# Optimization experiments

Measured on AMD Instinct MI355X. Metric: run time of the kernel, lower is better.

Reference implementation:

```python
import jax, jax.numpy as jnp
import numpy as np
from jax import lax

B, C_IN, C_OUT, H, W, K, PAD = 4, 64, 64, 96, 96, 3, 1
K2 = K * K


def setup_inputs() -> dict:
    key = jax.random.key(0)
    k1, k2, k3, k4, k5 = jax.random.split(key, 5)
    x = jax.random.normal(k1, (B, C_IN, H, W), jnp.float32)
    offset = jax.random.normal(k2, (B, 2 * K2, H, W), jnp.float32)
    weight = jax.random.normal(k3, (C_OUT, C_IN, K, K), jnp.float32) * 0.05
    mask_weight = jax.random.normal(k4, (K2, C_IN, K, K), jnp.float32) * 0.05
    mask_bias = jax.random.normal(k5, (K2,), jnp.float32) * 0.05
    return {"x": x, "offset": offset, "weight": weight,
            "mask_weight": mask_weight, "mask_bias": mask_bias}


def _deform_conv2d(x, offset, weight, mask):
    # torchvision ordering: per kernel tap k, offset[:, 2k] is dy, offset[:, 2k+1] is dx
    off_y = offset[:, 0::2]  # [B, K2, H, W]
    off_x = offset[:, 1::2]
    ky, kx = jnp.meshgrid(jnp.arange(K), jnp.arange(K), indexing="ij")
    ky = ky.reshape(K2).astype(x.dtype)
    kx = kx.reshape(K2).astype(x.dtype)
    hh = jnp.arange(H, dtype=x.dtype)
    ww = jnp.arange(W, dtype=x.dtype)
    base_y = hh[None, :, None] - PAD + ky[:, None, None]   # [K2, H, 1]
    base_x = ww[None, None, :] - PAD + kx[:, None, None]   # [K2, 1, W]
    py = base_y[None] + off_y                               # [B, K2, H, W]
    px = base_x[None] + off_x

    y0 = jnp.floor(py)
    x0 = jnp.floor(px)
    wy = py - y0   # bilinear weights
    wx = px - x0
    y0i = y0.astype(jnp.int32)
    x0i = x0.astype(jnp.int32)

    x_flat = x.reshape(B, C_IN, H * W)

    def gather(yy, xx):
        valid = (yy >= 0) & (yy < H) & (xx >= 0) & (xx < W)
        idx = jnp.clip(yy, 0, H - 1) * W + jnp.clip(xx, 0, W - 1)  # [B,K2,H,W]
        idx_f = idx.reshape(B, -1)
        v = jax.vmap(lambda xf, i: xf[:, i])(x_flat, idx_f)  # [B, C, K2*H*W]
        v = v.reshape(B, C_IN, K2, H, W)
        return v * valid[:, None].astype(v.dtype)

    v00 = gather(y0i, x0i)
    v01 = gather(y0i, x0i + 1)
    v10 = gather(y0i + 1, x0i)
    v11 = gather(y0i + 1, x0i + 1)

    wy_ = wy[:, None]  # [B,1,K2,H,W]
    wx_ = wx[:, None]
    sampled = (v00 * (1 - wy_) * (1 - wx_) + v01 * (1 - wy_) * wx_
               + v10 * wy_ * (1 - wx_) + v11 * wy_ * wx_)
    sampled = sampled * mask[:, None]  # modulate by sigmoid mask

    w2 = weight.reshape(C_OUT, C_IN, K2)
    return jnp.einsum("bckhw,ock->bohw", sampled, w2)


def reference(x, offset, weight, mask_weight, mask_bias):
    mask_logits = lax.conv_general_dilated(
        x, mask_weight, window_strides=(1, 1), padding=[(PAD, PAD), (PAD, PAD)],
        dimension_numbers=("NCHW", "OIHW", "NCHW"))
    mask = jax.nn.sigmoid(mask_logits + mask_bias[None, :, None, None])
    return _deform_conv2d(x, offset, weight, mask)
```

## Files before the change

### kernel.cpp

```cpp
#include <hip/hip_runtime.h>
#include <math.h>

#define BB 4
#define CI 64
#define CO 64
#define HH 96
#define WW 96
#define HW (HH*WW)
#define K2 9
#define NT (HW/64)
#define TPX 32
#define NTT (HW/TPX)
#define PADC 1

typedef __attribute__((ext_vector_type(8))) short short8;
typedef __attribute__((ext_vector_type(4))) float float4v;

#define XT_USHORTS ((size_t)BB*HW*64)
#define WF_USHORTS (18*64*32)
#define MWF_USHORTS (18*16*32)

__device__ __forceinline__ float bf2f(short s) {
    return __uint_as_float(((unsigned int)(unsigned short)s) << 16);
}
__device__ __forceinline__ short f2bf(float f) {
    unsigned int u = __float_as_uint(f);
    u = (u + 0x7fffu + ((u >> 16) & 1u)) >> 16;
    return (short)u;
}

__device__ __forceinline__ void unswz64(int bid, int* b, int* tile) {
    int g = bid & 7, r = bid >> 3;
    *b = g & 3;
    *tile = (g >> 2) * 72 + r;
}
__device__ __forceinline__ void unswz32(int bid, int* b, int* tile) {
    int g = bid & 7, r = bid >> 3;
    *b = g & 3;
    *tile = (g >> 2) * 144 + r;
}

__global__ __launch_bounds__(256) void prep_kernel(const float* __restrict__ x,
                                                   const float* __restrict__ wgt,
                                                   const float* __restrict__ mw,
                                                   unsigned short* __restrict__ xT,
                                                   unsigned short* __restrict__ Wf,
                                                   unsigned short* __restrict__ MWf) {
    __shared__ unsigned short ts[64][72];
    int t = threadIdx.x;
    if (blockIdx.x < BB * NT) {
        int b, tl; unswz64(blockIdx.x, &b, &tl);
        int p0 = tl * 64;
        const float* xb = x + (size_t)b * CI * HW + p0;
        int pq = t & 15, cg = t >> 4;
        #pragma unroll
        for (int i = 0; i < 4; i++) {
            int c = cg + i * 16;
            float4v v = *(const float4v*)(xb + (size_t)c * HW + pq * 4);
            ts[pq * 4 + 0][c] = (unsigned short)f2bf(v[0]);
            ts[pq * 4 + 1][c] = (unsigned short)f2bf(v[1]);
            ts[pq * 4 + 2][c] = (unsigned short)f2bf(v[2]);
            ts[pq * 4 + 3][c] = (unsigned short)f2bf(v[3]);
        }
        __syncthreads();
        int px = t >> 2, cq = t & 3;
        unsigned short* xo = xT + ((size_t)b * HW + p0 + px) * 64 + cq * 16;
        *(short8*)xo       = *(const short8*)&ts[px][cq * 16];
        *(short8*)(xo + 8) = *(const short8*)&ts[px][cq * 16 + 8];
    } else {
        int i = (blockIdx.x - BB * NT) * 256 + t;
        if (i < WF_USHORTS) {
            int frag = i >> 11;
            int o = (i >> 5) & 63;
            int tt = i & 31;
            int k = frag >> 1, cc = frag & 1;
            int c = cc * 32 + tt;
            Wf[i] = (unsigned short)f2bf(wgt[o * 576 + c * 9 + k]);
        } else if (i < WF_USHORTS + MWF_USHORTS) {
            int e = i - WF_USHORTS;
            int frag = e >> 9;
            int m = (e >> 5) & 15;
            int tt = e & 31;
            int q = frag >> 1, cc = frag & 1;
            int c = cc * 32 + tt;
            MWf[e] = (m < 9) ? (unsigned short)f2bf(mw[m * 576 + c * 9 + q]) : 0;
        }
    }
}

__global__ __launch_bounds__(256) void fused_kernel(const float* __restrict__ off,
                                                    const float* __restrict__ mbias,
                                                    const unsigned short* __restrict__ xT,
                                                    const unsigned short* __restrict__ Wf,
                                                    const unsigned short* __restrict__ MWf,
                                                    float* __restrict__ out) {
    __shared__ float s_mred[2][K2][TPX];
    __shared__ int   s_idx[K2][4][TPX];
    __shared__ float s_w[K2][4][TPX];
    __shared__ float s_part[2][16][64];

    int t = threadIdx.x;
    int lane = t & 63, wv = t >> 6;
    int pg = wv & 1, ch = wv >> 1;
    int n = lane & 15, quad = lane >> 4;
    int b, tl; unswz32(blockIdx.x, &b, &tl);
    int p0 = tl * TPX;
    int pxl = pg * 16 + n;
    int p = p0 + pxl;
    int h = p / WW, wc = p % WW;
    const unsigned short* xTb = xT + (size_t)b * HW * 64;
    int cbase = ch * 32 + quad * 8;

    {
        float4v macc = {0.f, 0.f, 0.f, 0.f};
        #pragma unroll
        for (int q = 0; q < 9; q++) {
            int hh = h + q / 3 - 1, ww2 = wc + q % 3 - 1;
            bool valid = (hh >= 0) && (hh < HH) && (ww2 >= 0) && (ww2 < WW);
            int nidx = valid ? (hh * WW + ww2) : 0;
            short8 bfrag = {0, 0, 0, 0, 0, 0, 0, 0};
            if (valid) bfrag = *(const short8*)(xTb + (size_t)nidx * 64 + cbase);
            short8 afrag = *(const short8*)(MWf + ((size_t)((q * 2 + ch) * 16 + n)) * 32 + quad * 8);
            macc = __builtin_amdgcn_mfma_f32_16x16x32_bf16(afrag, bfrag, macc, 0, 0, 0);
        }
        #pragma unroll
        for (int r = 0; r < 4; r++) {
            int row = quad * 4 + r;
            if (row < 9) s_mred[ch][row][pxl] = macc[r];
        }
    }
    __syncthreads();

    for (int e = t; e < K2 * TPX; e += 256) {
        int k = e >> 5, pe = e & 31;
        int pp = p0 + pe;
        int hh0 = pp / WW, ww0 = pp % WW;
        int ky = k / 3, kx = k % 3;
        float oy = off[((size_t)b * 2 * K2 + 2 * k) * HW + pp];
        float ox = off[((size_t)b * 2 * K2 + 2 * k + 1) * HW + pp];
        float s = s_mred[0][k][pe] + s_mred[1][k][pe] + mbias[k];
        float m = 1.f / (1.f + expf(-s));
        float py = (float)(hh0 - PADC + ky) + oy;
        float pxf = (float)(ww0 - PADC + kx) + ox;
        float y0f = floorf(py), x0f = floorf(pxf);
        float wy = py - y0f, wx = pxf - x0f;
        int y0 = (int)y0f, x0 = (int)x0f;
        int y1 = y0 + 1, x1 = x0 + 1;
        int y0c = min(max(y0, 0), HH - 1), y1c = min(max(y1, 0), HH - 1);
        int x0c = min(max(x0, 0), WW - 1), x1c = min(max(x1, 0), WW - 1);
        bool vy0 = (y0 >= 0) && (y0 < HH), vy1 = (y1 >= 0) && (y1 < HH);
        bool vx0 = (x0 >= 0) && (x0 < WW), vx1 = (x1 >= 0) && (x1 < WW);
        float w00 = (1.f - wy) * (1.f - wx) * m; if (!(vy0 && vx0)) w00 = 0.f;
        float w01 = (1.f - wy) * wx * m;         if (!(vy0 && vx1)) w01 = 0.f;
        float w10 = wy * (1.f - wx) * m;         if (!(vy1 && vx0)) w10 = 0.f;
        float w11 = wy * wx * m;                 if (!(vy1 && vx1)) w11 = 0.f;
        s_idx[k][0][pe] = y0c * WW + x0c;
        s_idx[k][1][pe] = y0c * WW + x1c;
        s_idx[k][2][pe] = y1c * WW + x0c;
        s_idx[k][3][pe] = y1c * WW + x1c;
        s_w[k][0][pe] = w00; s_w[k][1][pe] = w01;
        s_w[k][2][pe] = w10; s_w[k][3][pe] = w11;
    }
    __syncthreads();

    float4v acc0 = {0.f, 0.f, 0.f, 0.f};
    float4v acc1 = {0.f, 0.f, 0.f, 0.f};
    float4v acc2 = {0.f, 0.f, 0.f, 0.f};
    float4v acc3 = {0.f, 0.f, 0.f, 0.f};
    const unsigned short* xq = xTb + cbase;

    #pragma unroll
    for (int k = 0; k < 9; k++) {
        int i0 = s_idx[k][0][pxl], i1 = s_idx[k][1][pxl];
        int i2 = s_idx[k][2][pxl], i3 = s_idx[k][3][pxl];
        float w0 = s_w[k][0][pxl], w1 = s_w[k][1][pxl];
        float w2 = s_w[k][2][pxl], w3 = s_w[k][3][pxl];
        short8 u0 = *(const short8*)(xq + (size_t)i0 * 64);
        short8 u1 = *(const short8*)(xq + (size_t)i1 * 64);
        short8 u2 = *(const short8*)(xq + (size_t)i2 * 64);
        short8 u3 = *(const short8*)(xq + (size_t)i3 * 64);
        short8 bfrag;
        #pragma unroll
        for (int j = 0; j < 8; j++) {
            float v = bf2f(u0[j]) * w0 + bf2f(u1[j]) * w1 +
                      bf2f(u2[j]) * w2 + bf2f(u3[j]) * w3;
            bfrag[j] = f2bf(v);
        }
        const unsigned short* wp = Wf + (size_t)((k * 2 + ch) * 64) * 32 + quad * 8;
        short8 a0 = *(const short8*)(wp + (0 * 16 + n) * 32);
        short8 a1 = *(const short8*)(wp + (1 * 16 + n) * 32);
        short8 a2 = *(const short8*)(wp + (2 * 16 + n) * 32);
        short8 a3 = *(const short8*)(wp + (3 * 16 + n) * 32);
        acc0 = __builtin_amdgcn_mfma_f32_16x16x32_bf16(a0, bfrag, acc0, 0, 0, 0);
        acc1 = __builtin_amdgcn_mfma_f32_16x16x32_bf16(a1, bfrag, acc1, 0, 0, 0);
        acc2 = __builtin_amdgcn_mfma_f32_16x16x32_bf16(a2, bfrag, acc2, 0, 0, 0);
        acc3 = __builtin_amdgcn_mfma_f32_16x16x32_bf16(a3, bfrag, acc3, 0, 0, 0);
    }

    if (ch == 1) {
        #pragma unroll
        for (int r = 0; r < 4; r++) {
            s_part[pg][0 * 4 + r][lane] = acc0[r];
            s_part[pg][1 * 4 + r][lane] = acc1[r];
            s_part[pg][2 * 4 + r][lane] = acc2[r];
            s_part[pg][3 * 4 + r][lane] = acc3[r];
        }
    }
    __syncthreads();
    if (ch == 0) {
        float* ob = out + (size_t)b * CO * HW + p0 + pxl;
        #pragma unroll
        for (int r = 0; r < 4; r++) {
            ob[(size_t)(0 * 16 + quad * 4 + r) * HW] = acc0[r] + s_part[pg][0 * 4 + r][lane];
            ob[(size_t)(1 * 16 + quad * 4 + r) * HW] = acc1[r] + s_part[pg][1 * 4 + r][lane];
            ob[(size_t)(2 * 16 + quad * 4 + r) * HW] = acc2[r] + s_part[pg][2 * 4 + r][lane];
            ob[(size_t)(3 * 16 + quad * 4 + r) * HW] = acc3[r] + s_part[pg][3 * 4 + r][lane];
        }
    }
}

extern "C" void kernel_launch(void* const* d_in, const int* in_sizes, int n_in,
                              void* d_out, int out_size, void* d_ws, size_t ws_size,
                              hipStream_t stream) {
    const float* x   = (const float*)d_in[0];
    const float* off = (const float*)d_in[1];
    const float* wgt = (const float*)d_in[2];
    const float* mw  = (const float*)d_in[3];
    const float* mb  = (const float*)d_in[4];
    float* out = (float*)d_out;

    unsigned short* xT  = (unsigned short*)d_ws;
    unsigned short* Wf  = xT + XT_USHORTS;
    unsigned short* MWf = Wf + WF_USHORTS;

    int prep_grid = BB * NT + (WF_USHORTS + MWF_USHORTS + 255) / 256;
    hipLaunchKernelGGL(prep_kernel, dim3(prep_grid), dim3(256), 0, stream,
                       x, wgt, mw, xT, Wf, MWf);
    hipLaunchKernelGGL(fused_kernel, dim3(BB * NTT), dim3(256), 0, stream,
                       off, mb, xT, Wf, MWf, out);
}
```

Before: 112.1 us.

## Split kernel taps across waves with 16-pixel tiles and smaller prep tiles

```diff
diff --git a/kernel.cpp b/kernel.cpp
--- a/kernel.cpp
+++ b/kernel.cpp
@@ -8,9 +8,9 @@
 #define WW 96
 #define HW (HH*WW)
 #define K2 9
-#define NT (HW/64)
-#define TPX 32
+#define TPX 16
 #define NTT (HW/TPX)
+#define NTP 288
 #define PADC 1
 
 typedef __attribute__((ext_vector_type(8))) short short8;
@@ -29,10 +29,10 @@
     return (short)u;
 }
 
-__device__ __forceinline__ void unswz64(int bid, int* b, int* tile) {
+__device__ __forceinline__ void unswz16(int bid, int* b, int* tile) {
     int g = bid & 7, r = bid >> 3;
     *b = g & 3;
-    *tile = (g >> 2) * 72 + r;
+    *tile = (g >> 2) * 288 + r;
 }
 __device__ __forceinline__ void unswz32(int bid, int* b, int* tile) {
     int g = bid & 7, r = bid >> 3;
@@ -40,22 +40,23 @@
     *tile = (g >> 2) * 144 + r;
 }
 
+#define PBASE (BB*NTP)
 __global__ __launch_bounds__(256) void prep_kernel(const float* __restrict__ x,
                                                    const float* __restrict__ wgt,
                                                    const float* __restrict__ mw,
                                                    unsigned short* __restrict__ xT,
                                                    unsigned short* __restrict__ Wf,
                                                    unsigned short* __restrict__ MWf) {
-    __shared__ unsigned short ts[64][72];
+    __shared__ unsigned short ts[32][72];
     int t = threadIdx.x;
-    if (blockIdx.x < BB * NT) {
-        int b, tl; unswz64(blockIdx.x, &b, &tl);
-        int p0 = tl * 64;
+    if (blockIdx.x < PBASE) {
+        int b, tl; unswz32(blockIdx.x, &b, &tl);
+        int p0 = tl * 32;
         const float* xb = x + (size_t)b * CI * HW + p0;
-        int pq = t & 15, cg = t >> 4;
-        #pragma unroll
-        for (int i = 0; i < 4; i++) {
-            int c = cg + i * 16;
+        int c0 = t >> 3, pq = t & 7;
+        #pragma unroll
+        for (int i = 0; i < 2; i++) {
+            int c = c0 + i * 32;
             float4v v = *(const float4v*)(xb + (size_t)c * HW + pq * 4);
             ts[pq * 4 + 0][c] = (unsigned short)f2bf(v[0]);
             ts[pq * 4 + 1][c] = (unsigned short)f2bf(v[1]);
@@ -63,12 +64,11 @@
             ts[pq * 4 + 3][c] = (unsigned short)f2bf(v[3]);
         }
         __syncthreads();
-        int px = t >> 2, cq = t & 3;
-        unsigned short* xo = xT + ((size_t)b * HW + p0 + px) * 64 + cq * 16;
-        *(short8*)xo       = *(const short8*)&ts[px][cq * 16];
-        *(short8*)(xo + 8) = *(const short8*)&ts[px][cq * 16 + 8];
+        int px = t >> 3, cq = t & 7;
+        unsigned short* xo = xT + ((size_t)b * HW + p0 + px) * 64 + cq * 8;
+        *(short8*)xo = *(const short8*)&ts[px][cq * 8];
     } else {
-        int i = (blockIdx.x - BB * NT) * 256 + t;
+        int i = (blockIdx.x - PBASE) * 256 + t;
         if (i < WF_USHORTS) {
             int frag = i >> 11;
             int o = (i >> 5) & 63;
@@ -88,57 +88,60 @@
     }
 }
 
-__global__ __launch_bounds__(256) void fused_kernel(const float* __restrict__ off,
-                                                    const float* __restrict__ mbias,
-                                                    const unsigned short* __restrict__ xT,
-                                                    const unsigned short* __restrict__ Wf,
-                                                    const unsigned short* __restrict__ MWf,
-                                                    float* __restrict__ out) {
-    __shared__ float s_mred[2][K2][TPX];
+__global__ __launch_bounds__(256, 6) void fused_kernel(const float* __restrict__ off,
+                                                       const float* __restrict__ mbias,
+                                                       const unsigned short* __restrict__ xT,
+                                                       const unsigned short* __restrict__ Wf,
+                                                       const unsigned short* __restrict__ MWf,
+                                                       float* __restrict__ out) {
+    __shared__ float s_mred[2][2][K2][TPX];
     __shared__ int   s_idx[K2][4][TPX];
     __shared__ float s_w[K2][4][TPX];
-    __shared__ float s_part[2][16][64];
+    __shared__ float s_part[3][16][64];
 
     int t = threadIdx.x;
     int lane = t & 63, wv = t >> 6;
-    int pg = wv & 1, ch = wv >> 1;
+    int ch = wv & 1, tg = wv >> 1;
     int n = lane & 15, quad = lane >> 4;
-    int b, tl; unswz32(blockIdx.x, &b, &tl);
+    int b, tl; unswz16(blockIdx.x, &b, &tl);
     int p0 = tl * TPX;
-    int pxl = pg * 16 + n;
-    int p = p0 + pxl;
+    int p = p0 + n;
     int h = p / WW, wc = p % WW;
     const unsigned short* xTb = xT + (size_t)b * HW * 64;
     int cbase = ch * 32 + quad * 8;
 
     {
         float4v macc = {0.f, 0.f, 0.f, 0.f};
-        #pragma unroll
-        for (int q = 0; q < 9; q++) {
-            int hh = h + q / 3 - 1, ww2 = wc + q % 3 - 1;
-            bool valid = (hh >= 0) && (hh < HH) && (ww2 >= 0) && (ww2 < WW);
-            int nidx = valid ? (hh * WW + ww2) : 0;
-            short8 bfrag = {0, 0, 0, 0, 0, 0, 0, 0};
-            if (valid) bfrag = *(const short8*)(xTb + (size_t)nidx * 64 + cbase);
-            short8 afrag = *(const short8*)(MWf + ((size_t)((q * 2 + ch) * 16 + n)) * 32 + quad * 8);
-            macc = __builtin_amdgcn_mfma_f32_16x16x32_bf16(afrag, bfrag, macc, 0, 0, 0);
-        }
+#define PHASE_A(QB, QE)                                                          \
+        _Pragma("unroll")                                                        \
+        for (int q = QB; q < QE; q++) {                                          \
+            int hh = h + q / 3 - 1, ww2 = wc + q % 3 - 1;                        \
+            bool valid = (hh >= 0) && (hh < HH) && (ww2 >= 0) && (ww2 < WW);     \
+            int nidx = valid ? (hh * WW + ww2) : 0;                              \
+            short8 bfrag = {0, 0, 0, 0, 0, 0, 0, 0};                             \
+            if (valid) bfrag = *(const short8*)(xTb + (size_t)nidx * 64 + cbase);\
+            short8 afrag = *(const short8*)(MWf +                                \
+                ((size_t)((q * 2 + ch) * 16 + n)) * 32 + quad * 8);              \
+            macc = __builtin_amdgcn_mfma_f32_16x16x32_bf16(afrag, bfrag, macc, 0, 0, 0); \
+        }
+        if (tg == 0) { PHASE_A(0, 5) } else { PHASE_A(5, 9) }
         #pragma unroll
         for (int r = 0; r < 4; r++) {
             int row = quad * 4 + r;
-            if (row < 9) s_mred[ch][row][pxl] = macc[r];
+            if (row < 9) s_mred[ch][tg][row][n] = macc[r];
         }
     }
     __syncthreads();
 
-    for (int e = t; e < K2 * TPX; e += 256) {
-        int k = e >> 5, pe = e & 31;
+    if (t < K2 * TPX) {
+        int k = t >> 4, pe = t & 15;
         int pp = p0 + pe;
         int hh0 = pp / WW, ww0 = pp % WW;
         int ky = k / 3, kx = k % 3;
         float oy = off[((size_t)b * 2 * K2 + 2 * k) * HW + pp];
         float ox = off[((size_t)b * 2 * K2 + 2 * k + 1) * HW + pp];
-        float s = s_mred[0][k][pe] + s_mred[1][k][pe] + mbias[k];
+        float s = s_mred[0][0][k][pe] + s_mred[0][1][k][pe] +
+                  s_mred[1][0][k][pe] + s_mred[1][1][k][pe] + mbias[k];
         float m = 1.f / (1.f + expf(-s));
         float py = (float)(hh0 - PADC + ky) + oy;
         float pxf = (float)(ww0 - PADC + kx) + ox;
@@ -169,52 +172,59 @@
     float4v acc3 = {0.f, 0.f, 0.f, 0.f};
     const unsigned short* xq = xTb + cbase;
 
-    #pragma unroll
-    for (int k = 0; k < 9; k++) {
-        int i0 = s_idx[k][0][pxl], i1 = s_idx[k][1][pxl];
-        int i2 = s_idx[k][2][pxl], i3 = s_idx[k][3][pxl];
-        float w0 = s_w[k][0][pxl], w1 = s_w[k][1][pxl];
-        float w2 = s_w[k][2][pxl], w3 = s_w[k][3][pxl];
-        short8 u0 = *(const short8*)(xq + (size_t)i0 * 64);
-        short8 u1 = *(const short8*)(xq + (size_t)i1 * 64);
-        short8 u2 = *(const short8*)(xq + (size_t)i2 * 64);
-        short8 u3 = *(const short8*)(xq + (size_t)i3 * 64);
-        short8 bfrag;
-        #pragma unroll
-        for (int j = 0; j < 8; j++) {
-            float v = bf2f(u0[j]) * w0 + bf2f(u1[j]) * w1 +
-                      bf2f(u2[j]) * w2 + bf2f(u3[j]) * w3;
-            bfrag[j] = f2bf(v);
-        }
-        const unsigned short* wp = Wf + (size_t)((k * 2 + ch) * 64) * 32 + quad * 8;
-        short8 a0 = *(const short8*)(wp + (0 * 16 + n) * 32);
-        short8 a1 = *(const short8*)(wp + (1 * 16 + n) * 32);
-        short8 a2 = *(const short8*)(wp + (2 * 16 + n) * 32);
-        short8 a3 = *(const short8*)(wp + (3 * 16 + n) * 32);
-        acc0 = __builtin_amdgcn_mfma_f32_16x16x32_bf16(a0, bfrag, acc0, 0, 0, 0);
-        acc1 = __builtin_amdgcn_mfma_f32_16x16x32_bf16(a1, bfrag, acc1, 0, 0, 0);
-        acc2 = __builtin_amdgcn_mfma_f32_16x16x32_bf16(a2, bfrag, acc2, 0, 0, 0);
-        acc3 = __builtin_amdgcn_mfma_f32_16x16x32_bf16(a3, bfrag, acc3, 0, 0, 0);
-    }
-
-    if (ch == 1) {
+#define PHASE_C(KB, KE)                                                          \
+    _Pragma("unroll")                                                            \
+    for (int k = KB; k < KE; k++) {                                              \
+        int i0 = s_idx[k][0][n], i1 = s_idx[k][1][n];                            \
+        int i2 = s_idx[k][2][n], i3 = s_idx[k][3][n];                            \
+        float w0 = s_w[k][0][n], w1 = s_w[k][1][n];                              \
+        float w2 = s_w[k][2][n], w3 = s_w[k][3][n];                              \
+        short8 u0 = *(const short8*)(xq + (size_t)i0 * 64);                      \
+        short8 u1 = *(const short8*)(xq + (size_t)i1 * 64);                      \
+        short8 u2 = *(const short8*)(xq + (size_t)i2 * 64);                      \
+        short8 u3 = *(const short8*)(xq + (size_t)i3 * 64);                      \
+        short8 bfrag;                                                            \
+        _Pragma("unroll")                                                        \
+        for (int j = 0; j < 8; j++) {                                            \
+            float v = bf2f(u0[j]) * w0 + bf2f(u1[j]) * w1 +                      \
+                      bf2f(u2[j]) * w2 + bf2f(u3[j]) * w3;                       \
+            bfrag[j] = f2bf(v);                                                  \
+        }                                                                        \
+        const unsigned short* wp = Wf + (size_t)((k * 2 + ch) * 64) * 32 + quad * 8; \
+        short8 a0 = *(const short8*)(wp + (0 * 16 + n) * 32);                    \
+        short8 a1 = *(const short8*)(wp + (1 * 16 + n) * 32);                    \
+        short8 a2 = *(const short8*)(wp + (2 * 16 + n) * 32);                    \
+        short8 a3 = *(const short8*)(wp + (3 * 16 + n) * 32);                    \
+        acc0 = __builtin_amdgcn_mfma_f32_16x16x32_bf16(a0, bfrag, acc0, 0, 0, 0);\
+        acc1 = __builtin_amdgcn_mfma_f32_16x16x32_bf16(a1, bfrag, acc1, 0, 0, 0);\
+        acc2 = __builtin_amdgcn_mfma_f32_16x16x32_bf16(a2, bfrag, acc2, 0, 0, 0);\
+        acc3 = __builtin_amdgcn_mfma_f32_16x16x32_bf16(a3, bfrag, acc3, 0, 0, 0);\
+    }
+    if (tg == 0) { PHASE_C(0, 5) } else { PHASE_C(5, 9) }
+
+    if (wv != 0) {
         #pragma unroll
         for (int r = 0; r < 4; r++) {
-            s_part[pg][0 * 4 + r][lane] = acc0[r];
-            s_part[pg][1 * 4 + r][lane] = acc1[r];
-            s_part[pg][2 * 4 + r][lane] = acc2[r];
-            s_part[pg][3 * 4 + r][lane] = acc3[r];
+            s_part[wv - 1][0 * 4 + r][lane] = acc0[r];
+            s_part[wv - 1][1 * 4 + r][lane] = acc1[r];
+            s_part[wv - 1][2 * 4 + r][lane] = acc2[r];
+            s_part[wv - 1][3 * 4 + r][lane] = acc3[r];
         }
     }
     __syncthreads();
-    if (ch == 0) {
-        float* ob = out + (size_t)b * CO * HW + p0 + pxl;
+    if (wv == 0) {
+        float* ob = out + (size_t)b * CO * HW + p0 + n;
         #pragma unroll
         for (int r = 0; r < 4; r++) {
-            ob[(size_t)(0 * 16 + quad * 4 + r) * HW] = acc0[r] + s_part[pg][0 * 4 + r][lane];
-            ob[(size_t)(1 * 16 + quad * 4 + r) * HW] = acc1[r] + s_part[pg][1 * 4 + r][lane];
-            ob[(size_t)(2 * 16 + quad * 4 + r) * HW] = acc2[r] + s_part[pg][2 * 4 + r][lane];
-            ob[(size_t)(3 * 16 + quad * 4 + r) * HW] = acc3[r] + s_part[pg][3 * 4 + r][lane];
+            int j0 = 0 * 4 + r, j1 = 1 * 4 + r, j2 = 2 * 4 + r, j3 = 3 * 4 + r;
+            ob[(size_t)(0 * 16 + quad * 4 + r) * HW] =
+                acc0[r] + s_part[0][j0][lane] + s_part[1][j0][lane] + s_part[2][j0][lane];
+            ob[(size_t)(1 * 16 + quad * 4 + r) * HW] =
+                acc1[r] + s_part[0][j1][lane] + s_part[1][j1][lane] + s_part[2][j1][lane];
+            ob[(size_t)(2 * 16 + quad * 4 + r) * HW] =
+                acc2[r] + s_part[0][j2][lane] + s_part[1][j2][lane] + s_part[2][j2][lane];
+            ob[(size_t)(3 * 16 + quad * 4 + r) * HW] =
+                acc3[r] + s_part[0][j3][lane] + s_part[1][j3][lane] + s_part[2][j3][lane];
         }
     }
 }
@@ -233,7 +243,7 @@
     unsigned short* Wf  = xT + XT_USHORTS;
     unsigned short* MWf = Wf + WF_USHORTS;
 
-    int prep_grid = BB * NT + (WF_USHORTS + MWF_USHORTS + 255) / 256;
+    int prep_grid = PBASE + (WF_USHORTS + MWF_USHORTS + 255) / 256;
     hipLaunchKernelGGL(prep_kernel, dim3(prep_grid), dim3(256), 0, stream,
                        x, wgt, mw, xT, Wf, MWf);
     hipLaunchKernelGGL(fused_kernel, dim3(BB * NTT), dim3(256), 0, stream,
```

After: 106.8 us. 1.05x faster.

## Stage bf16 input halo window in LDS per 2D tile, drop transpose pass

Applied to the files above, without the earlier changes.

```diff
diff --git a/kernel.cpp b/kernel.cpp
--- a/kernel.cpp
+++ b/kernel.cpp
@@ -8,15 +8,24 @@
 #define WW 96
 #define HW (HH*WW)
 #define K2 9
-#define NT (HW/64)
-#define TPX 32
-#define NTT (HW/TPX)
 #define PADC 1
+
+#define TW 8
+#define TH 4
+#define TPXT (TW*TH)
+#define TBX (WW/TW)
+#define TBY (HH/TH)
+#define NTILB (TBX*TBY)
+#define NTILES (BB*NTILB)
+
+#define WR (TH+9)
+#define WC 20
+#define SREC 72
+#define NSLOT (WR*WC)
 
 typedef __attribute__((ext_vector_type(8))) short short8;
 typedef __attribute__((ext_vector_type(4))) float float4v;
 
-#define XT_USHORTS ((size_t)BB*HW*64)
 #define WF_USHORTS (18*64*32)
 #define MWF_USHORTS (18*16*32)
 
@@ -29,97 +38,101 @@
     return (short)u;
 }
 
-__device__ __forceinline__ void unswz64(int bid, int* b, int* tile) {
+__device__ __forceinline__ void unswz(int bid, int* b, int* ty, int* tx) {
     int g = bid & 7, r = bid >> 3;
     *b = g & 3;
-    *tile = (g >> 2) * 72 + r;
-}
-__device__ __forceinline__ void unswz32(int bid, int* b, int* tile) {
-    int g = bid & 7, r = bid >> 3;
-    *b = g & 3;
-    *tile = (g >> 2) * 144 + r;
-}
-
-__global__ __launch_bounds__(256) void prep_kernel(const float* __restrict__ x,
-                                                   const float* __restrict__ wgt,
+    int tile = (g >> 2) * 144 + r;
+    *ty = tile / TBX; *tx = tile % TBX;
+}
+
+__global__ __launch_bounds__(256) void pack_kernel(const float* __restrict__ wgt,
                                                    const float* __restrict__ mw,
-                                                   unsigned short* __restrict__ xT,
                                                    unsigned short* __restrict__ Wf,
                                                    unsigned short* __restrict__ MWf) {
-    __shared__ unsigned short ts[64][72];
-    int t = threadIdx.x;
-    if (blockIdx.x < BB * NT) {
-        int b, tl; unswz64(blockIdx.x, &b, &tl);
-        int p0 = tl * 64;
-        const float* xb = x + (size_t)b * CI * HW + p0;
-        int pq = t & 15, cg = t >> 4;
-        #pragma unroll
-        for (int i = 0; i < 4; i++) {
-            int c = cg + i * 16;
-            float4v v = *(const float4v*)(xb + (size_t)c * HW + pq * 4);
-            ts[pq * 4 + 0][c] = (unsigned short)f2bf(v[0]);
-            ts[pq * 4 + 1][c] = (unsigned short)f2bf(v[1]);
-            ts[pq * 4 + 2][c] = (unsigned short)f2bf(v[2]);
-            ts[pq * 4 + 3][c] = (unsigned short)f2bf(v[3]);
-        }
-        __syncthreads();
-        int px = t >> 2, cq = t & 3;
-        unsigned short* xo = xT + ((size_t)b * HW + p0 + px) * 64 + cq * 16;
-        *(short8*)xo       = *(const short8*)&ts[px][cq * 16];
-        *(short8*)(xo + 8) = *(const short8*)&ts[px][cq * 16 + 8];
-    } else {
-        int i = (blockIdx.x - BB * NT) * 256 + t;
-        if (i < WF_USHORTS) {
-            int frag = i >> 11;
-            int o = (i >> 5) & 63;
-            int tt = i & 31;
-            int k = frag >> 1, cc = frag & 1;
-            int c = cc * 32 + tt;
-            Wf[i] = (unsigned short)f2bf(wgt[o * 576 + c * 9 + k]);
-        } else if (i < WF_USHORTS + MWF_USHORTS) {
-            int e = i - WF_USHORTS;
-            int frag = e >> 9;
-            int m = (e >> 5) & 15;
-            int tt = e & 31;
-            int q = frag >> 1, cc = frag & 1;
-            int c = cc * 32 + tt;
-            MWf[e] = (m < 9) ? (unsigned short)f2bf(mw[m * 576 + c * 9 + q]) : 0;
-        }
-    }
-}
-
-__global__ __launch_bounds__(256) void fused_kernel(const float* __restrict__ off,
-                                                    const float* __restrict__ mbias,
-                                                    const unsigned short* __restrict__ xT,
-                                                    const unsigned short* __restrict__ Wf,
-                                                    const unsigned short* __restrict__ MWf,
-                                                    float* __restrict__ out) {
-    __shared__ float s_mred[2][K2][TPX];
-    __shared__ int   s_idx[K2][4][TPX];
-    __shared__ float s_w[K2][4][TPX];
-    __shared__ float s_part[2][16][64];
+    int i = blockIdx.x * 256 + threadIdx.x;
+    if (i < WF_USHORTS) {
+        int frag = i >> 11;
+        int o = (i >> 5) & 63;
+        int tt = i & 31;
+        int k = frag >> 1, cc = frag & 1;
+        int c = cc * 32 + tt;
+        Wf[i] = (unsigned short)f2bf(wgt[o * 576 + c * 9 + k]);
+    } else if (i < WF_USHORTS + MWF_USHORTS) {
+        int e = i - WF_USHORTS;
+        int frag = e >> 9;
+        int m = (e >> 5) & 15;
+        int tt = e & 31;
+        int q = frag >> 1, cc = frag & 1;
+        int c = cc * 32 + tt;
+        MWf[e] = (m < 9) ? (unsigned short)f2bf(mw[m * 576 + c * 9 + q]) : 0;
+    }
+}
+
+__global__ __launch_bounds__(256, 3) void fused_kernel(const float* __restrict__ x,
+                                                       const float* __restrict__ off,
+                                                       const float* __restrict__ mbias,
+                                                       const unsigned short* __restrict__ Wf,
+                                                       const unsigned short* __restrict__ MWf,
+                                                       float* __restrict__ out) {
+    __shared__ __align__(16) unsigned short win[NSLOT * SREC];
+    __shared__ float s_mred[2][K2][TPXT];
+    __shared__ int   s_idx[K2][4][TPXT];
+    __shared__ float s_w[K2][4][TPXT];
+    float* part = (float*)win;
 
     int t = threadIdx.x;
     int lane = t & 63, wv = t >> 6;
-    int pg = wv & 1, ch = wv >> 1;
+    int pg = wv >> 1, ch = wv & 1;
     int n = lane & 15, quad = lane >> 4;
-    int b, tl; unswz32(blockIdx.x, &b, &tl);
-    int p0 = tl * TPX;
+    int b, ty, tx; unswz(blockIdx.x, &b, &ty, &tx);
+    int h0 = ty * TH, w0 = tx * TW;
+    int wr0 = h0 - 4, wc0 = w0 - 4;
+    const float* xb = x + (size_t)b * CI * HW;
+
+    for (int e = t; e < WR * 32 * 5; e += 256) {
+        int r = e / 160, rem = e % 160, chp = rem / 5, c4 = rem % 5;
+        int row = min(max(wr0 + r, 0), HH - 1);
+        int c0c = wc0 + c4 * 4;
+        const float* s0 = xb + (size_t)(2 * chp) * HW + row * WW;
+        const float* s1 = s0 + HW;
+        float v0[4], v1[4];
+        if (c0c >= 0 && c0c + 3 < WW) {
+            float4v a = *(const float4v*)(s0 + c0c);
+            float4v bq = *(const float4v*)(s1 + c0c);
+            v0[0]=a[0]; v0[1]=a[1]; v0[2]=a[2]; v0[3]=a[3];
+            v1[0]=bq[0]; v1[1]=bq[1]; v1[2]=bq[2]; v1[3]=bq[3];
+        } else {
+            #pragma unroll
+            for (int j = 0; j < 4; j++) {
+                int cc2 = min(max(c0c + j, 0), WW - 1);
+                v0[j] = s0[cc2]; v1[j] = s1[cc2];
+            }
+        }
+        #pragma unroll
+        for (int j = 0; j < 4; j++) {
+            unsigned int pk = (unsigned short)f2bf(v0[j]) |
+                              ((unsigned int)(unsigned short)f2bf(v1[j]) << 16);
+            *(unsigned int*)&win[(r * WC + c4 * 4 + j) * SREC + 2 * chp] = pk;
+        }
+    }
+    __syncthreads();
+
     int pxl = pg * 16 + n;
-    int p = p0 + pxl;
-    int h = p / WW, wc = p % WW;
-    const unsigned short* xTb = xT + (size_t)b * HW * 64;
-    int cbase = ch * 32 + quad * 8;
+    int ly = pxl >> 3, lx = pxl & 7;
+    int h = h0 + ly, wcc = w0 + lx;
+    int cbase_us = ch * 32 + quad * 8;
 
     {
         float4v macc = {0.f, 0.f, 0.f, 0.f};
         #pragma unroll
         for (int q = 0; q < 9; q++) {
-            int hh = h + q / 3 - 1, ww2 = wc + q % 3 - 1;
+            int hh = h + q / 3 - 1, ww2 = wcc + q % 3 - 1;
             bool valid = (hh >= 0) && (hh < HH) && (ww2 >= 0) && (ww2 < WW);
-            int nidx = valid ? (hh * WW + ww2) : 0;
             short8 bfrag = {0, 0, 0, 0, 0, 0, 0, 0};
-            if (valid) bfrag = *(const short8*)(xTb + (size_t)nidx * 64 + cbase);
+            if (valid) {
+                int slot = (hh - wr0) * WC + (ww2 - wc0);
+                bfrag = *(const short8*)&win[slot * SREC + cbase_us];
+            }
             short8 afrag = *(const short8*)(MWf + ((size_t)((q * 2 + ch) * 16 + n)) * 32 + quad * 8);
             macc = __builtin_amdgcn_mfma_f32_16x16x32_bf16(afrag, bfrag, macc, 0, 0, 0);
         }
@@ -131,17 +144,16 @@
     }
     __syncthreads();
 
-    for (int e = t; e < K2 * TPX; e += 256) {
+    for (int e = t; e < K2 * TPXT; e += 256) {
         int k = e >> 5, pe = e & 31;
-        int pp = p0 + pe;
-        int hh0 = pp / WW, ww0 = pp % WW;
-        int ky = k / 3, kx = k % 3;
-        float oy = off[((size_t)b * 2 * K2 + 2 * k) * HW + pp];
-        float ox = off[((size_t)b * 2 * K2 + 2 * k + 1) * HW + pp];
+        int ph = h0 + (pe >> 3), pw = w0 + (pe & 7);
+        int p = ph * WW + pw;
+        float oy = off[((size_t)b * 2 * K2 + 2 * k) * HW + p];
+        float ox = off[((size_t)b * 2 * K2 + 2 * k + 1) * HW + p];
         float s = s_mred[0][k][pe] + s_mred[1][k][pe] + mbias[k];
         float m = 1.f / (1.f + expf(-s));
-        float py = (float)(hh0 - PADC + ky) + oy;
-        float pxf = (float)(ww0 - PADC + kx) + ox;
+        float py  = (float)(ph - PADC + k / 3) + oy;
+        float pxf = (float)(pw - PADC + k % 3) + ox;
         float y0f = floorf(py), x0f = floorf(pxf);
         float wy = py - y0f, wx = pxf - x0f;
         int y0 = (int)y0f, x0 = (int)x0f;
@@ -154,10 +166,10 @@
         float w01 = (1.f - wy) * wx * m;         if (!(vy0 && vx1)) w01 = 0.f;
         float w10 = wy * (1.f - wx) * m;         if (!(vy1 && vx0)) w10 = 0.f;
         float w11 = wy * wx * m;                 if (!(vy1 && vx1)) w11 = 0.f;
-        s_idx[k][0][pe] = y0c * WW + x0c;
-        s_idx[k][1][pe] = y0c * WW + x1c;
-        s_idx[k][2][pe] = y1c * WW + x0c;
-        s_idx[k][3][pe] = y1c * WW + x1c;
+        s_idx[k][0][pe] = (y0c << 16) | x0c;
+        s_idx[k][1][pe] = (y0c << 16) | x1c;
+        s_idx[k][2][pe] = (y1c << 16) | x0c;
+        s_idx[k][3][pe] = (y1c << 16) | x1c;
         s_w[k][0][pe] = w00; s_w[k][1][pe] = w01;
         s_w[k][2][pe] = w10; s_w[k][3][pe] = w11;
     }
@@ -167,23 +179,34 @@
     float4v acc1 = {0.f, 0.f, 0.f, 0.f};
     float4v acc2 = {0.f, 0.f, 0.f, 0.f};
     float4v acc3 = {0.f, 0.f, 0.f, 0.f};
-    const unsigned short* xq = xTb + cbase;
+    const float* xfb = xb + (size_t)(ch * 32 + quad * 8) * HW;
 
     #pragma unroll
     for (int k = 0; k < 9; k++) {
-        int i0 = s_idx[k][0][pxl], i1 = s_idx[k][1][pxl];
-        int i2 = s_idx[k][2][pxl], i3 = s_idx[k][3][pxl];
+        short8 U[4];
+        #pragma unroll
+        for (int cor = 0; cor < 4; cor++) {
+            int yx = s_idx[k][cor][pxl];
+            int yy = yx >> 16, xx = yx & 0xffff;
+            int r = yy - wr0, c = xx - wc0;
+            bool inw = ((unsigned)r < (unsigned)WR) && ((unsigned)c < (unsigned)WC);
+            short8 u;
+            if (inw) {
+                u = *(const short8*)&win[(r * WC + c) * SREC + cbase_us];
+            } else {
+                const float* fs = xfb + yy * WW + xx;
+                #pragma unroll
+                for (int j = 0; j < 8; j++) u[j] = f2bf(fs[(size_t)j * HW]);
+            }
+            U[cor] = u;
+        }
         float w0 = s_w[k][0][pxl], w1 = s_w[k][1][pxl];
         float w2 = s_w[k][2][pxl], w3 = s_w[k][3][pxl];
-        short8 u0 = *(const short8*)(xq + (size_t)i0 * 64);
-        short8 u1 = *(const short8*)(xq + (size_t)i1 * 64);
-        short8 u2 = *(const short8*)(xq + (size_t)i2 * 64);
-        short8 u3 = *(const short8*)(xq + (size_t)i3 * 64);
         short8 bfrag;
         #pragma unroll
         for (int j = 0; j < 8; j++) {
-            float v = bf2f(u0[j]) * w0 + bf2f(u1[j]) * w1 +
-                      bf2f(u2[j]) * w2 + bf2f(u3[j]) * w3;
+            float v = bf2f(U[0][j]) * w0 + bf2f(U[1][j]) * w1 +
+                      bf2f(U[2][j]) * w2 + bf2f(U[3][j]) * w3;
             bfrag[j] = f2bf(v);
         }
         const unsigned short* wp = Wf + (size_t)((k * 2 + ch) * 64) * 32 + quad * 8;
@@ -197,24 +220,29 @@
         acc3 = __builtin_amdgcn_mfma_f32_16x16x32_bf16(a3, bfrag, acc3, 0, 0, 0);
     }
 
+    __syncthreads();
     if (ch == 1) {
         #pragma unroll
         for (int r = 0; r < 4; r++) {
-            s_part[pg][0 * 4 + r][lane] = acc0[r];
-            s_part[pg][1 * 4 + r][lane] = acc1[r];
-            s_part[pg][2 * 4 + r][lane] = acc2[r];
-            s_part[pg][3 * 4 + r][lane] = acc3[r];
+            part[(pg * 16 + 0 * 4 + r) * 64 + lane] = acc0[r];
+            part[(pg * 16 + 1 * 4 + r) * 64 + lane] = acc1[r];
+            part[(pg * 16 + 2 * 4 + r) * 64 + lane] = acc2[r];
+            part[(pg * 16 + 3 * 4 + r) * 64 + lane] = acc3[r];
         }
     }
     __syncthreads();
     if (ch == 0) {
-        float* ob = out + (size_t)b * CO * HW + p0 + pxl;
+        float* ob = out + (size_t)b * CO * HW + h * WW + wcc;
         #pragma unroll
         for (int r = 0; r < 4; r++) {
-            ob[(size_t)(0 * 16 + quad * 4 + r) * HW] = acc0[r] + s_part[pg][0 * 4 + r][lane];
-            ob[(size_t)(1 * 16 + quad * 4 + r) * HW] = acc1[r] + s_part[pg][1 * 4 + r][lane];
-            ob[(size_t)(2 * 16 + quad * 4 + r) * HW] = acc2[r] + s_part[pg][2 * 4 + r][lane];
-            ob[(size_t)(3 * 16 + quad * 4 + r) * HW] = acc3[r] + s_part[pg][3 * 4 + r][lane];
+            ob[(size_t)(0 * 16 + quad * 4 + r) * HW] =
+                acc0[r] + part[(pg * 16 + 0 * 4 + r) * 64 + lane];
+            ob[(size_t)(1 * 16 + quad * 4 + r) * HW] =
+                acc1[r] + part[(pg * 16 + 1 * 4 + r) * 64 + lane];
+            ob[(size_t)(2 * 16 + quad * 4 + r) * HW] =
+                acc2[r] + part[(pg * 16 + 2 * 4 + r) * 64 + lane];
+            ob[(size_t)(3 * 16 + quad * 4 + r) * HW] =
+                acc3[r] + part[(pg * 16 + 3 * 4 + r) * 64 + lane];
         }
     }
 }
@@ -229,13 +257,11 @@
     const float* mb  = (const float*)d_in[4];
     float* out = (float*)d_out;
 
-    unsigned short* xT  = (unsigned short*)d_ws;
-    unsigned short* Wf  = xT + XT_USHORTS;
+    unsigned short* Wf  = (unsigned short*)d_ws;
     unsigned short* MWf = Wf + WF_USHORTS;
 
-    int prep_grid = BB * NT + (WF_USHORTS + MWF_USHORTS + 255) / 256;
-    hipLaunchKernelGGL(prep_kernel, dim3(prep_grid), dim3(256), 0, stream,
-                       x, wgt, mw, xT, Wf, MWf);
-    hipLaunchKernelGGL(fused_kernel, dim3(BB * NTT), dim3(256), 0, stream,
-                       off, mb, xT, Wf, MWf, out);
-}
+    hipLaunchKernelGGL(pack_kernel, dim3((WF_USHORTS + MWF_USHORTS + 255) / 256), dim3(256),
+                       0, stream, wgt, mw, Wf, MWf);
+    hipLaunchKernelGGL(fused_kernel, dim3(NTILES), dim3(256), 0, stream,
+                       x, off, mb, Wf, MWf, out);
+}
```

Result: faster. 101.2 us (-9.7%).
